# Kernel optimization log

Measured on AMD Instinct MI355X. Metric: run time of the kernel, lower is better.

## Reference

```python
import jax, jax.numpy as jnp
import numpy as np
import itertools, math

B = 2048
DIM = 384
RES = 7
KEY_DIM = 16
HEADS = 8
RATIO = 4
NH_KD = KEY_DIM * HEADS          # 128
D = RATIO * KEY_DIM              # 64
DH = D * HEADS                   # 512
OUT_DIM = DIM                    # 384
RES2 = math.ceil(RES / 2)        # 4
N = RES * RES                    # 49
N2 = RES2 * RES2                 # 16
EPS = 1e-5
SCALE = KEY_DIM ** -0.5


def conv2d(x, w, b, stride=1, pad=0, groups=1):
    out = jax.lax.conv_general_dilated(
        x, w, (stride, stride), [(pad, pad), (pad, pad)],
        dimension_numbers=("NCHW", "OIHW", "NCHW"), feature_group_count=groups)
    return out + b[None, :, None, None]


def bn(x, p):
    # p: [4, C] = (gamma, beta, running_mean, running_var); inference-mode BN
    g, be, m, v = p[0], p[1], p[2], p[3]
    inv = jax.lax.rsqrt(v + EPS)
    return (x - m[None, :, None, None]) * (g * inv)[None, :, None, None] + be[None, :, None, None]


def avgpool2(x):
    # AvgPool2d(kernel=2, stride=2, padding=0)
    s = jax.lax.reduce_window(x, 0.0, jax.lax.add, (1, 1, 2, 2), (1, 1, 2, 2), "VALID")
    return s * 0.25


def _bias_idxs():
    points = list(itertools.product(range(RES), range(RES)))
    points_ = list(itertools.product(range(RES2), range(RES2)))
    stride = RES / RES2
    offsets, idxs = {}, []
    for p1 in points_:
        for p2 in points:
            off = (math.floor(abs(p1[0] * stride - p2[0])),
                   math.floor(abs(p1[1] * stride - p2[1])))
            if off not in offsets:
                offsets[off] = len(offsets)
            idxs.append(offsets[off])
    return np.array(idxs, dtype=np.int32).reshape(N2, N), len(offsets)


def _bn_params(k, c):
    k1, k2, k3, k4 = jax.random.split(k, 4)
    gamma = 1.0 + 0.1 * jax.random.normal(k1, (c,), jnp.float32)
    beta = 0.1 * jax.random.normal(k2, (c,), jnp.float32)
    mean = 0.1 * jax.random.normal(k3, (c,), jnp.float32)
    var = jax.random.uniform(k4, (c,), jnp.float32, 0.5, 1.5)
    return jnp.stack([gamma, beta, mean, var])


def _conv_w(k, shape):
    fan_in = shape[1] * shape[2] * shape[3]
    return jax.random.normal(k, shape, jnp.float32) / np.sqrt(fan_in)


def setup_inputs() -> dict:
    key = jax.random.key(0)
    ks = jax.random.split(key, 20)
    idxs_np, n_off = _bias_idxs()
    inp = {
        "x": jax.random.normal(ks[0], (B, DIM, RES, RES), jnp.float32),
        # LGQuery: depthwise 3x3 s2 + proj 1x1 + BN
        "qlw": _conv_w(ks[1], (DIM, 1, 3, 3)),
        "qlb": 0.01 * jax.random.normal(ks[2], (DIM,), jnp.float32),
        "qpw": _conv_w(ks[3], (NH_KD, DIM, 1, 1)),
        "qpb": 0.01 * jax.random.normal(ks[4], (NH_KD,), jnp.float32),
        "qbn": _bn_params(ks[5], NH_KD),
        # K branch: 1x1 conv + BN
        "kw": _conv_w(ks[6], (NH_KD, DIM, 1, 1)),
        "kb": 0.01 * jax.random.normal(ks[7], (NH_KD,), jnp.float32),
        "kbn": _bn_params(ks[8], NH_KD),
        # V branch: 1x1 conv + BN
        "vw": _conv_w(ks[9], (DH, DIM, 1, 1)),
        "vb": 0.01 * jax.random.normal(ks[10], (DH,), jnp.float32),
        "vbn": _bn_params(ks[11], DH),
        # v_local: depthwise 3x3 s2 + BN
        "vlw": _conv_w(ks[12], (DH, 1, 3, 3)),
        "vlb": 0.01 * jax.random.normal(ks[13], (DH,), jnp.float32),
        "vlbn": _bn_params(ks[14], DH),
        # proj: ReLU -> 1x1 conv -> BN
        "pw": _conv_w(ks[15], (OUT_DIM, DH, 1, 1)),
        "pb": 0.01 * jax.random.normal(ks[16], (OUT_DIM,), jnp.float32),
        "pbn": _bn_params(ks[17], OUT_DIM),
        # relative position biases + gather indices
        "ab": 0.02 * jax.random.normal(ks[18], (HEADS, n_off), jnp.float32),
        "bias_idxs": jnp.asarray(idxs_np),
    }
    return inp


def reference(x, qlw, qlb, qpw, qpb, qbn, kw, kb, kbn, vw, vb, vbn,
              vlw, vlb, vlbn, pw, pb, pbn, ab, bias_idxs):
    Bx = x.shape[0]
    # --- LGQuery ---
    local_q = conv2d(x, qlw, qlb, stride=2, pad=1, groups=DIM)   # [B,384,4,4]
    pool_q = avgpool2(x)                                         # [B,384,3,3]
    ph = local_q.shape[-2] - pool_q.shape[-2]
    pw_ = local_q.shape[-1] - pool_q.shape[-1]
    if ph > 0 or pw_ > 0:
        pool_q = jnp.pad(pool_q, ((0, 0), (0, 0), (0, ph), (0, pw_)))
    q_out = bn(conv2d(local_q + pool_q, qpw, qpb), qbn)          # [B,128,4,4]
    Hq, Wq = q_out.shape[-2], q_out.shape[-1]
    Nq = Hq * Wq
    # --- K / V ---
    k_out = bn(conv2d(x, kw, kb), kbn)                           # [B,128,7,7]
    Nk = k_out.shape[-2] * k_out.shape[-1]
    v_out = bn(conv2d(x, vw, vb), vbn)                           # [B,512,7,7]
    v_loc = bn(conv2d(v_out, vlw, vlb, stride=2, pad=1, groups=DH), vlbn)  # [B,512,4,4]
    # --- attention over tiny 16x49 matrices per head ---
    q = q_out.reshape(Bx, HEADS, KEY_DIM, Nq)                    # [B,H,kd,Nq]
    k = k_out.reshape(Bx, HEADS, KEY_DIM, Nk)                    # [B,H,kd,Nk]
    v = v_out.reshape(Bx, HEADS, D, Nk)                          # [B,H,d,Nk]
    attn = jnp.einsum("bhdq,bhdk->bhqk", q, k) * SCALE           # [B,H,16,49]
    if Nq == N2 and Nk == N:
        attn = attn + ab[:, bias_idxs]                           # gather -> [H,16,49]
    attn = jax.nn.softmax(attn, axis=-1)
    xa = jnp.einsum("bhqk,bhdk->bhdq", attn, v)                  # [B,H,d,Nq]
    out = xa.reshape(Bx, DH, Hq, Wq)                             # [B,512,4,4]
    ph2 = out.shape[-2] - v_loc.shape[-2]
    pw2 = out.shape[-1] - v_loc.shape[-1]
    if ph2 > 0 or pw2 > 0:
        v_loc = jnp.pad(v_loc, ((0, 0), (0, 0), (0, ph2), (0, pw2)))
    out = out + v_loc
    out = bn(conv2d(jax.nn.relu(out), pw, pb), pbn)              # [B,384,4,4]
    return out
```

## Files before the change

### kernel.cpp

```cpp
#include <hip/hip_runtime.h>
#include <hip/hip_bf16.h>


#define DIMC 384
#define NPOS 49
#define NHKD 128
#define DHC  512
#define OUTC 384

#define OFF_KW  0
#define OFF_VW  49152
#define OFF_QPW 245760
#define OFF_PW  294912
#define W_TOT   491520

#define XS_OFF 0
#define R0_OFF 19208
#define R1_OFF 27528
#define R2_OFF 32648
#define SMEM_ELEMS 40840

typedef __attribute__((ext_vector_type(8))) __bf16 bf16x8;
typedef __attribute__((ext_vector_type(4))) float f32x4;

static __device__ __forceinline__ __hip_bfloat16 f2b(float x) { return __float2bfloat16(x); }
static __device__ __forceinline__ float b2f(__hip_bfloat16 x) { return __bfloat162float(x); }
static __device__ __forceinline__ bf16x8 ld8(const __hip_bfloat16* p) { return *(const bf16x8*)p; }
static __device__ __forceinline__ f32x4 fzero() {
  f32x4 z; z[0] = 0.f; z[1] = 0.f; z[2] = 0.f; z[3] = 0.f; return z;
}
static __device__ __forceinline__ bf16x8 bzero() {
  bf16x8 z;
  #pragma unroll
  for (int j = 0; j < 8; ++j) z[j] = (__bf16)0.0f;
  return z;
}

static __device__ __forceinline__ void bn_so(const float* bn, int C, int ch,
                                             float convb, float& s, float& o) {
  float g  = bn[ch];
  float be = bn[C + ch];
  float mu = bn[2*C + ch];
  float va = bn[3*C + ch];
  s = g * rsqrtf(va + 1e-5f);
  o = be + (convb - mu) * s;
}

__global__ void prep_weights(const float* __restrict__ kw, const float* __restrict__ vw,
                             const float* __restrict__ qpw, const float* __restrict__ pw,
                             __hip_bfloat16* __restrict__ wsb) {
  for (int i = blockIdx.x * blockDim.x + threadIdx.x; i < W_TOT; i += gridDim.x * blockDim.x) {
    float v;
    if (i < OFF_VW)       v = kw[i - OFF_KW];
    else if (i < OFF_QPW) v = vw[i - OFF_VW];
    else if (i < OFF_PW)  v = qpw[i - OFF_QPW];
    else                  v = pw[i - OFF_PW];
    wsb[i] = f2b(v);
  }
}

__global__ __launch_bounds__(512, 4) void attn4d_kernel(
    const float* __restrict__ x,
    const float* __restrict__ qlw, const float* __restrict__ qlb,
    const float* __restrict__ qpb, const float* __restrict__ qbn,
    const float* __restrict__ kb,  const float* __restrict__ kbn,
    const float* __restrict__ vb,  const float* __restrict__ vbn,
    const float* __restrict__ vlw, const float* __restrict__ vlb,
    const float* __restrict__ vlbn,
    const float* __restrict__ pb,  const float* __restrict__ pbn,
    const float* __restrict__ ab,  const int* __restrict__ bidx,
    const __hip_bfloat16* __restrict__ wsb,
    int n_off, float* __restrict__ out)
{
  __shared__ __align__(16) __hip_bfloat16 smem[SMEM_ELEMS];
  __hip_bfloat16* xs    = smem + XS_OFF;
  __hip_bfloat16* vsm   = smem + XS_OFF;
  __hip_bfloat16* kt    = smem + R0_OFF;
  __hip_bfloat16* rout  = smem + R0_OFF;
  __hip_bfloat16* qsm   = smem + R1_OFF;
  __hip_bfloat16* qin   = smem + R2_OFF;
  __hip_bfloat16* attnS = smem + R2_OFF;

  const __hip_bfloat16* kwb  = wsb + OFF_KW;
  const __hip_bfloat16* vwb  = wsb + OFF_VW;
  const __hip_bfloat16* qpwb = wsb + OFF_QPW;
  const __hip_bfloat16* pwb  = wsb + OFF_PW;

  const int tid  = threadIdx.x;
  const int lane = tid & 63;
  const int wave = tid >> 6;
  const int quad = lane >> 4;
  const int l15  = lane & 15;
  const int b    = blockIdx.x;

  {
    const float* xg = x + (size_t)b * (DIMC * NPOS);
    for (int j = tid; j < NPOS * (DIMC / 8); j += 512) {
      const int n  = j % 49;
      const int c0 = (j / 49) * 8;
      union { bf16x8 v; __hip_bfloat16 h[8]; } u;
      #pragma unroll
      for (int k = 0; k < 8; ++k)
        u.h[k] = f2b(xg[(c0 + k) * 49 + n]);
      *(bf16x8*)&xs[n * 392 + c0] = u.v;
    }
  }
  __syncthreads();

  if (tid < DIMC) {
    const int c = tid;
    float xv[49];
    #pragma unroll
    for (int n = 0; n < 49; ++n) xv[n] = b2f(xs[n * 392 + c]);
    float wq[9];
    #pragma unroll
    for (int j = 0; j < 9; ++j) wq[j] = qlw[c * 9 + j];
    const float cb = qlb[c];
    #pragma unroll
    for (int oh = 0; oh < 4; ++oh) {
      #pragma unroll
      for (int ow = 0; ow < 4; ++ow) {
        float a = cb;
        #pragma unroll
        for (int kh = 0; kh < 3; ++kh) {
          const int ih = 2 * oh - 1 + kh;
          if (ih < 0 || ih > 6) continue;
          #pragma unroll
          for (int kwi = 0; kwi < 3; ++kwi) {
            const int iw = 2 * ow - 1 + kwi;
            if (iw < 0 || iw > 6) continue;
            a += wq[kh * 3 + kwi] * xv[ih * 7 + iw];
          }
        }
        if (oh < 3 && ow < 3)
          a += 0.25f * (xv[(2*oh)*7 + 2*ow] + xv[(2*oh)*7 + 2*ow + 1] +
                        xv[(2*oh+1)*7 + 2*ow] + xv[(2*oh+1)*7 + 2*ow + 1]);
        qin[(oh * 4 + ow) * 392 + c] = f2b(a);
      }
    }
  }
  __syncthreads();


  {
    const int mt = wave;
    f32x4 acc[4];
    #pragma unroll
    for (int nt = 0; nt < 4; ++nt) acc[nt] = fzero();
    for (int ks = 0; ks < 12; ++ks) {
      const int c0 = ks * 32 + quad * 8;
      bf16x8 a = ld8(&kwb[(mt * 16 + l15) * DIMC + c0]);
      bf16x8 z[4];
      #pragma unroll
      for (int nt = 0; nt < 3; ++nt) z[nt] = ld8(&xs[(nt * 16 + l15) * 392 + c0]);
      z[3] = (l15 == 0) ? ld8(&xs[48 * 392 + c0]) : bzero();
      #pragma unroll
      for (int nt = 0; nt < 4; ++nt)
        acc[nt] = __builtin_amdgcn_mfma_f32_16x16x32_bf16(a, z[nt], acc[nt], 0, 0, 0);
    }
    #pragma unroll
    for (int r = 0; r < 4; ++r) {
      const int oc = mt * 16 + quad * 4 + r;
      float s, o;
      bn_so(kbn, NHKD, oc, kb[oc], s, o);
      #pragma unroll
      for (int nt = 0; nt < 4; ++nt) {
        const int n = nt * 16 + l15;
        if (n < 49) kt[n * 136 + oc] = f2b(acc[nt][r] * s + o);
      }
    }
  }

  {
    const int mt = wave;
    f32x4 acc = fzero();
    for (int ks = 0; ks < 12; ++ks) {
      const int c0 = ks * 32 + quad * 8;
      bf16x8 bv = ld8(&qin[l15 * 392 + c0]);
      bf16x8 av = ld8(&qpwb[(mt * 16 + l15) * DIMC + c0]);
      acc = __builtin_amdgcn_mfma_f32_16x16x32_bf16(av, bv, acc, 0, 0, 0);
    }
    #pragma unroll
    for (int r = 0; r < 4; ++r) {
      const int oc = mt * 16 + quad * 4 + r;
      float s, o;
      bn_so(qbn, NHKD, oc, qpb[oc], s, o);
      const int kd = oc & 15;
      qsm[wave * 640 + l15 * 40 + kd] = f2b(acc[r] * s + o);
      qsm[wave * 640 + l15 * 40 + kd + 16] = f2b(0.f);
    }
  }

  f32x4 va[2][2][4];
  #pragma unroll
  for (int p = 0; p < 2; ++p)
    #pragma unroll
    for (int mt = 0; mt < 2; ++mt)
      #pragma unroll
      for (int nt = 0; nt < 4; ++nt) va[p][mt][nt] = fzero();
  {
    const int chb = wave * 32;
    for (int ks = 0; ks < 12; ++ks) {
      const int c0 = ks * 32 + quad * 8;
      bf16x8 z[4];
      #pragma unroll
      for (int nt = 0; nt < 3; ++nt) z[nt] = ld8(&xs[(nt * 16 + l15) * 392 + c0]);
      z[3] = (l15 == 0) ? ld8(&xs[48 * 392 + c0]) : bzero();
      #pragma unroll
      for (int p = 0; p < 2; ++p) {
        #pragma unroll
        for (int mt = 0; mt < 2; ++mt) {
          bf16x8 a = ld8(&vwb[(p * 256 + chb + mt * 16 + l15) * DIMC + c0]);
          #pragma unroll
          for (int nt = 0; nt < 4; ++nt)
            va[p][mt][nt] = __builtin_amdgcn_mfma_f32_16x16x32_bf16(a, z[nt], va[p][mt][nt], 0, 0, 0);
        }
      }
    }
  }
  __syncthreads();

  {
    __hip_bfloat16* vbw_ = vsm + wave * 2304;
    #pragma unroll
    for (int mt = 0; mt < 2; ++mt)
      #pragma unroll
      for (int r = 0; r < 4; ++r) {
        const int chl = mt * 16 + quad * 4 + r;
        const int gch = wave * 32 + chl;
        float s, o;
        bn_so(vbn, DHC, gch, vb[gch], s, o);
        #pragma unroll
        for (int nt = 0; nt < 4; ++nt)
          vbw_[chl * 72 + nt * 16 + l15] = f2b(va[0][mt][nt][r] * s + o);
      }
  }

  {
    const int h = wave;
    bf16x8 av = ld8(&qsm[h * 640 + l15 * 40 + quad * 8]);
    float p[4][4];
    #pragma unroll
    for (int t = 0; t < 4; ++t) {
      bf16x8 bv = bzero();
      if (quad < 2) bv = ld8(&kt[(t * 16 + l15) * 136 + h * 16 + quad * 8]);
      f32x4 lg = __builtin_amdgcn_mfma_f32_16x16x32_bf16(av, bv, fzero(), 0, 0, 0);
      #pragma unroll
      for (int r = 0; r < 4; ++r) {
        const int nq = quad * 4 + r;
        const int nk = t * 16 + l15;
        float val = -30000.f;
        if (nk < 49) val = lg[r] * 0.25f + ab[h * n_off + bidx[nq * 49 + nk]];
        p[t][r] = val;
      }
    }
    #pragma unroll
    for (int r = 0; r < 4; ++r) {
      float m = fmaxf(fmaxf(p[0][r], p[1][r]), fmaxf(p[2][r], p[3][r]));
      m = fmaxf(m, __shfl_xor(m, 1));
      m = fmaxf(m, __shfl_xor(m, 2));
      m = fmaxf(m, __shfl_xor(m, 4));
      m = fmaxf(m, __shfl_xor(m, 8));
      float e[4], sum = 0.f;
      #pragma unroll
      for (int t = 0; t < 4; ++t) { e[t] = __expf(p[t][r] - m); sum += e[t]; }
      sum += __shfl_xor(sum, 1);
      sum += __shfl_xor(sum, 2);
      sum += __shfl_xor(sum, 4);
      sum += __shfl_xor(sum, 8);
      const float inv = 1.f / sum;
      #pragma unroll
      for (int t = 0; t < 4; ++t) p[t][r] = e[t] * inv;
    }
    #pragma unroll
    for (int r = 0; r < 4; ++r) {
      const int nq = quad * 4 + r;
      #pragma unroll
      for (int t = 0; t < 4; ++t) {
        const int nk = t * 16 + l15;
        attnS[h * 1024 + nq * 64 + (nk ^ ((nq & 7) << 3))] = f2b(p[t][r]);
      }
    }
  }
  __syncthreads();

  #pragma unroll
  for (int p = 0; p < 2; ++p) {
    if (p == 1) {
      __hip_bfloat16* vbw_ = vsm + wave * 2304;
      #pragma unroll
      for (int mt = 0; mt < 2; ++mt)
        #pragma unroll
        for (int r = 0; r < 4; ++r) {
          const int chl = mt * 16 + quad * 4 + r;
          const int gch = 256 + wave * 32 + chl;
          float s, o;
          bn_so(vbn, DHC, gch, vb[gch], s, o);
          #pragma unroll
          for (int nt = 0; nt < 4; ++nt)
            vbw_[chl * 72 + nt * 16 + l15] = f2b(va[1][mt][nt][r] * s + o);
        }
    }

    {
      const int cl   = lane & 31;
      const int half = lane >> 5;
      const int gch  = p * 256 + wave * 32 + cl;
      const __hip_bfloat16* vrow = vsm + wave * 2304 + cl * 72;
      float wv[9];
      #pragma unroll
      for (int j = 0; j < 9; ++j) wv[j] = vlw[gch * 9 + j];
      float s, o;
      bn_so(vlbn, DHC, gch, vlb[gch], s, o);
      #pragma unroll
      for (int pp = 0; pp < 8; ++pp) {
        const int pos = half * 8 + pp;
        const int oh = pos >> 2, ow = pos & 3;
        float a = 0.f;
        #pragma unroll
        for (int kh = 0; kh < 3; ++kh) {
          const int ih = 2 * oh - 1 + kh;
          if (ih < 0 || ih > 6) continue;
          #pragma unroll
          for (int kwi = 0; kwi < 3; ++kwi) {
            const int iw = 2 * ow - 1 + kwi;
            if (iw < 0 || iw > 6) continue;
            a += wv[kh * 3 + kwi] * b2f(vrow[ih * 7 + iw]);
          }
        }
        rout[pos * 520 + gch] = f2b(a * s + o);
      }
    }

    {
      const int h = p * 4 + (wave >> 1);
      const __hip_bfloat16* vbw_ = vsm + wave * 2304;
      #pragma unroll
      for (int mt = 0; mt < 2; ++mt) {
        f32x4 acc = fzero();
        #pragma unroll
        for (int ks = 0; ks < 2; ++ks) {
          const int k0 = ks * 32 + quad * 8;
          bf16x8 av = ld8(&vbw_[(mt * 16 + l15) * 72 + k0]);
          bf16x8 bv = ld8(&attnS[h * 1024 + l15 * 64 + (k0 ^ ((l15 & 7) << 3))]);
          acc = __builtin_amdgcn_mfma_f32_16x16x32_bf16(av, bv, acc, 0, 0, 0);
        }
        #pragma unroll
        for (int r = 0; r < 4; ++r) {
          const int gch = p * 256 + wave * 32 + mt * 16 + quad * 4 + r;
          const int ad = l15 * 520 + gch;
          const float val = acc[r] + b2f(rout[ad]);
          rout[ad] = f2b(fmaxf(val, 0.f));
        }
      }
    }
  }
  __syncthreads();

  {
    const int mt0 = wave * 3;
    f32x4 acc[3];
    #pragma unroll
    for (int t = 0; t < 3; ++t) acc[t] = fzero();
    for (int ks = 0; ks < 16; ++ks) {
      const int c0 = ks * 32 + quad * 8;
      bf16x8 bv = ld8(&rout[l15 * 520 + c0]);
      #pragma unroll
      for (int t = 0; t < 3; ++t) {
        bf16x8 av = ld8(&pwb[((mt0 + t) * 16 + l15) * DHC + c0]);
        acc[t] = __builtin_amdgcn_mfma_f32_16x16x32_bf16(av, bv, acc[t], 0, 0, 0);
      }
    }
    float* outb = out + (size_t)b * (OUTC * 16);
    #pragma unroll
    for (int t = 0; t < 3; ++t) {
      #pragma unroll
      for (int r = 0; r < 4; ++r) {
        const int oc = (mt0 + t) * 16 + quad * 4 + r;
        float s, o;
        bn_so(pbn, OUTC, oc, pb[oc], s, o);
        outb[oc * 16 + l15] = acc[t][r] * s + o;
      }
    }
  }
}

extern "C" void kernel_launch(void* const* d_in, const int* in_sizes, int n_in,
                              void* d_out, int out_size, void* d_ws, size_t ws_size,
                              hipStream_t stream) {
  const float* x    = (const float*)d_in[0];
  const float* qlw  = (const float*)d_in[1];
  const float* qlb  = (const float*)d_in[2];
  const float* qpw  = (const float*)d_in[3];
  const float* qpb  = (const float*)d_in[4];
  const float* qbn  = (const float*)d_in[5];
  const float* kw   = (const float*)d_in[6];
  const float* kb   = (const float*)d_in[7];
  const float* kbn  = (const float*)d_in[8];
  const float* vw   = (const float*)d_in[9];
  const float* vb   = (const float*)d_in[10];
  const float* vbn  = (const float*)d_in[11];
  const float* vlw  = (const float*)d_in[12];
  const float* vlb  = (const float*)d_in[13];
  const float* vlbn = (const float*)d_in[14];
  const float* pw   = (const float*)d_in[15];
  const float* pb   = (const float*)d_in[16];
  const float* pbn  = (const float*)d_in[17];
  const float* ab   = (const float*)d_in[18];
  const int*   bidx = (const int*)d_in[19];
  const int n_off = in_sizes[18] / 8;
  const int Bn = in_sizes[0] / (DIMC * NPOS);

  __hip_bfloat16* wsb = (__hip_bfloat16*)d_ws;

  prep_weights<<<480, 256, 0, stream>>>(kw, vw, qpw, pw, wsb);
  attn4d_kernel<<<Bn, 512, 0, stream>>>(x, qlw, qlb, qpb, qbn, kb, kbn,
                                        vb, vbn, vlw, vlb, vlbn, pb, pbn,
                                        ab, bidx, wsb, n_off, (float*)d_out);
}
```

Before: 580.2 us.

## Double block to 1024 threads, repartition GEMMs, precompute BN scale/offset tables

Raises the per-sample block from 512 to 1024 threads and redistributes every stage (q-path conv split by rows, K/V projections split across n-tiles and channel groups, attention on waves 8-15 overlapping with the v-local depthwise conv, output projection over 16 waves). All of V is kept in a separate, larger shared-memory region so the two-pass V handling goes away. BN scale/offset pairs are folded once in the prep kernel and stored in the workspace, replacing per-thread rsqrt and loads. Shared memory grows to about 156 KB per block, which limits residency to one block per CU and may reduce latency hiding.

```diff
diff --git a/kernel.cpp b/kernel.cpp
--- a/kernel.cpp
+++ b/kernel.cpp
@@ -13,12 +13,19 @@
 #define OFF_QPW 245760
 #define OFF_PW  294912
 #define W_TOT   491520
-
-#define XS_OFF 0
-#define R0_OFF 19208
-#define R1_OFF 27528
-#define R2_OFF 32648
-#define SMEM_ELEMS 40840
+#define BN_K  0
+#define BN_Q  128
+#define BN_V  256
+#define BN_VL 768
+#define BN_P  1280
+#define BN_TOT 1664
+
+#define XS_OFF   0
+#define KT_OFF   19208
+#define QSM_OFF  27912
+#define QIN_OFF  33032
+#define VSM_OFF  41224
+#define SMEM_ELEMS 78088
 
 typedef __attribute__((ext_vector_type(8))) __bf16 bf16x8;
 typedef __attribute__((ext_vector_type(4))) float f32x4;
@@ -36,20 +43,17 @@
   return z;
 }
 
-static __device__ __forceinline__ void bn_so(const float* bn, int C, int ch,
-                                             float convb, float& s, float& o) {
-  float g  = bn[ch];
-  float be = bn[C + ch];
-  float mu = bn[2*C + ch];
-  float va = bn[3*C + ch];
-  s = g * rsqrtf(va + 1e-5f);
-  o = be + (convb - mu) * s;
-}
-
 __global__ void prep_weights(const float* __restrict__ kw, const float* __restrict__ vw,
                              const float* __restrict__ qpw, const float* __restrict__ pw,
+                             const float* __restrict__ kb,  const float* __restrict__ kbn,
+                             const float* __restrict__ qpb, const float* __restrict__ qbn,
+                             const float* __restrict__ vb,  const float* __restrict__ vbn,
+                             const float* __restrict__ vlb, const float* __restrict__ vlbn,
+                             const float* __restrict__ pb,  const float* __restrict__ pbn,
                              __hip_bfloat16* __restrict__ wsb) {
-  for (int i = blockIdx.x * blockDim.x + threadIdx.x; i < W_TOT; i += gridDim.x * blockDim.x) {
+  const int gid = blockIdx.x * blockDim.x + threadIdx.x;
+  const int stride = gridDim.x * blockDim.x;
+  for (int i = gid; i < W_TOT; i += stride) {
     float v;
     if (i < OFF_VW)       v = kw[i - OFF_KW];
     else if (i < OFF_QPW) v = vw[i - OFF_VW];
@@ -57,34 +61,42 @@
     else                  v = pw[i - OFF_PW];
     wsb[i] = f2b(v);
   }
-}
-
-__global__ __launch_bounds__(512, 4) void attn4d_kernel(
+  float2* bnt = (float2*)(wsb + W_TOT);
+  for (int i = gid; i < BN_TOT; i += stride) {
+    const float *bn, *cb; int ch, C;
+    if (i < BN_Q)        { bn = kbn;  cb = kb;  ch = i;         C = NHKD; }
+    else if (i < BN_V)   { bn = qbn;  cb = qpb; ch = i - BN_Q;  C = NHKD; }
+    else if (i < BN_VL)  { bn = vbn;  cb = vb;  ch = i - BN_V;  C = DHC;  }
+    else if (i < BN_P)   { bn = vlbn; cb = vlb; ch = i - BN_VL; C = DHC;  }
+    else                 { bn = pbn;  cb = pb;  ch = i - BN_P;  C = OUTC; }
+    const float g = bn[ch], be = bn[C + ch], mu = bn[2*C + ch], va = bn[3*C + ch];
+    const float s = g * rsqrtf(va + 1e-5f);
+    bnt[i] = make_float2(s, be + (cb[ch] - mu) * s);
+  }
+}
+
+__global__ __launch_bounds__(1024, 4) void attn4d_kernel(
     const float* __restrict__ x,
     const float* __restrict__ qlw, const float* __restrict__ qlb,
-    const float* __restrict__ qpb, const float* __restrict__ qbn,
-    const float* __restrict__ kb,  const float* __restrict__ kbn,
-    const float* __restrict__ vb,  const float* __restrict__ vbn,
-    const float* __restrict__ vlw, const float* __restrict__ vlb,
-    const float* __restrict__ vlbn,
-    const float* __restrict__ pb,  const float* __restrict__ pbn,
+    const float* __restrict__ vlw,
     const float* __restrict__ ab,  const int* __restrict__ bidx,
     const __hip_bfloat16* __restrict__ wsb,
     int n_off, float* __restrict__ out)
 {
   __shared__ __align__(16) __hip_bfloat16 smem[SMEM_ELEMS];
   __hip_bfloat16* xs    = smem + XS_OFF;
-  __hip_bfloat16* vsm   = smem + XS_OFF;
-  __hip_bfloat16* kt    = smem + R0_OFF;
-  __hip_bfloat16* rout  = smem + R0_OFF;
-  __hip_bfloat16* qsm   = smem + R1_OFF;
-  __hip_bfloat16* qin   = smem + R2_OFF;
-  __hip_bfloat16* attnS = smem + R2_OFF;
+  __hip_bfloat16* rout  = smem + XS_OFF;
+  __hip_bfloat16* kt    = smem + KT_OFF;
+  __hip_bfloat16* qsm   = smem + QSM_OFF;
+  __hip_bfloat16* qin   = smem + QIN_OFF;
+  __hip_bfloat16* attnS = smem + QIN_OFF;
+  __hip_bfloat16* vsm   = smem + VSM_OFF;
 
   const __hip_bfloat16* kwb  = wsb + OFF_KW;
   const __hip_bfloat16* vwb  = wsb + OFF_VW;
   const __hip_bfloat16* qpwb = wsb + OFF_QPW;
   const __hip_bfloat16* pwb  = wsb + OFF_PW;
+  const float2* bnt = (const float2*)(wsb + W_TOT);
 
   const int tid  = threadIdx.x;
   const int lane = tid & 63;
@@ -95,7 +107,7 @@
 
   {
     const float* xg = x + (size_t)b * (DIMC * NPOS);
-    for (int j = tid; j < NPOS * (DIMC / 8); j += 512) {
+    for (int j = tid; j < NPOS * (DIMC / 8); j += 1024) {
       const int n  = j % 49;
       const int c0 = (j / 49) * 8;
       union { bf16x8 v; __hip_bfloat16 h[8]; } u;
@@ -107,17 +119,20 @@
   }
   __syncthreads();
 
-  if (tid < DIMC) {
-    const int c = tid;
-    float xv[49];
-    #pragma unroll
-    for (int n = 0; n < 49; ++n) xv[n] = b2f(xs[n * 392 + c]);
+  if (tid < 768) {
+    const int part = tid >= 384;
+    const int c    = tid - part * 384;
+    const int nb   = part * 21;
+    float xv[28];
+    #pragma unroll
+    for (int i = 0; i < 28; ++i) xv[i] = b2f(xs[(nb + i) * 392 + c]);
     float wq[9];
     #pragma unroll
     for (int j = 0; j < 9; ++j) wq[j] = qlw[c * 9 + j];
     const float cb = qlb[c];
     #pragma unroll
-    for (int oh = 0; oh < 4; ++oh) {
+    for (int ohh = 0; ohh < 2; ++ohh) {
+      const int oh = part * 2 + ohh;
       #pragma unroll
       for (int ow = 0; ow < 4; ++ow) {
         float a = cb;
@@ -129,12 +144,12 @@
           for (int kwi = 0; kwi < 3; ++kwi) {
             const int iw = 2 * ow - 1 + kwi;
             if (iw < 0 || iw > 6) continue;
-            a += wq[kh * 3 + kwi] * xv[ih * 7 + iw];
+            a += wq[kh * 3 + kwi] * xv[ih * 7 + iw - nb];
           }
         }
         if (oh < 3 && ow < 3)
-          a += 0.25f * (xv[(2*oh)*7 + 2*ow] + xv[(2*oh)*7 + 2*ow + 1] +
-                        xv[(2*oh+1)*7 + 2*ow] + xv[(2*oh+1)*7 + 2*ow + 1]);
+          a += 0.25f * (xv[(2*oh)*7 + 2*ow - nb]   + xv[(2*oh)*7 + 2*ow + 1 - nb] +
+                        xv[(2*oh+1)*7 + 2*ow - nb] + xv[(2*oh+1)*7 + 2*ow + 1 - nb]);
         qin[(oh * 4 + ow) * 392 + c] = f2b(a);
       }
     }
@@ -143,35 +158,30 @@
 
 
   {
-    const int mt = wave;
-    f32x4 acc[4];
-    #pragma unroll
-    for (int nt = 0; nt < 4; ++nt) acc[nt] = fzero();
+    const int nt  = wave & 3;
+    const int mtp = wave >> 2;
+    const int n   = nt * 16 + l15;
+    f32x4 acc[2]; acc[0] = fzero(); acc[1] = fzero();
     for (int ks = 0; ks < 12; ++ks) {
       const int c0 = ks * 32 + quad * 8;
-      bf16x8 a = ld8(&kwb[(mt * 16 + l15) * DIMC + c0]);
-      bf16x8 z[4];
-      #pragma unroll
-      for (int nt = 0; nt < 3; ++nt) z[nt] = ld8(&xs[(nt * 16 + l15) * 392 + c0]);
-      z[3] = (l15 == 0) ? ld8(&xs[48 * 392 + c0]) : bzero();
-      #pragma unroll
-      for (int nt = 0; nt < 4; ++nt)
-        acc[nt] = __builtin_amdgcn_mfma_f32_16x16x32_bf16(a, z[nt], acc[nt], 0, 0, 0);
-    }
-    #pragma unroll
-    for (int r = 0; r < 4; ++r) {
-      const int oc = mt * 16 + quad * 4 + r;
-      float s, o;
-      bn_so(kbn, NHKD, oc, kb[oc], s, o);
-      #pragma unroll
-      for (int nt = 0; nt < 4; ++nt) {
-        const int n = nt * 16 + l15;
-        if (n < 49) kt[n * 136 + oc] = f2b(acc[nt][r] * s + o);
-      }
-    }
-  }
-
-  {
+      bf16x8 z = (n < 49) ? ld8(&xs[n * 392 + c0]) : bzero();
+      #pragma unroll
+      for (int i = 0; i < 2; ++i) {
+        bf16x8 a = ld8(&kwb[((mtp * 2 + i) * 16 + l15) * DIMC + c0]);
+        acc[i] = __builtin_amdgcn_mfma_f32_16x16x32_bf16(a, z, acc[i], 0, 0, 0);
+      }
+    }
+    #pragma unroll
+    for (int i = 0; i < 2; ++i)
+      #pragma unroll
+      for (int r = 0; r < 4; ++r) {
+        const int oc = (mtp * 2 + i) * 16 + quad * 4 + r;
+        const float2 so = bnt[BN_K + oc];
+        if (n < 49) kt[n * 136 + oc] = f2b(acc[i][r] * so.x + so.y);
+      }
+  }
+
+  if (wave < 8) {
     const int mt = wave;
     f32x4 acc = fzero();
     for (int ks = 0; ks < 12; ++ks) {
@@ -183,61 +193,42 @@
     #pragma unroll
     for (int r = 0; r < 4; ++r) {
       const int oc = mt * 16 + quad * 4 + r;
-      float s, o;
-      bn_so(qbn, NHKD, oc, qpb[oc], s, o);
+      const float2 so = bnt[BN_Q + oc];
       const int kd = oc & 15;
-      qsm[wave * 640 + l15 * 40 + kd] = f2b(acc[r] * s + o);
+      qsm[wave * 640 + l15 * 40 + kd] = f2b(acc[r] * so.x + so.y);
       qsm[wave * 640 + l15 * 40 + kd + 16] = f2b(0.f);
     }
   }
 
-  f32x4 va[2][2][4];
-  #pragma unroll
-  for (int p = 0; p < 2; ++p)
-    #pragma unroll
-    for (int mt = 0; mt < 2; ++mt)
-      #pragma unroll
-      for (int nt = 0; nt < 4; ++nt) va[p][mt][nt] = fzero();
-  {
-    const int chb = wave * 32;
+  {
+    const int nt   = wave >> 2;
+    const int mgrp = wave & 3;
+    const int n    = nt * 16 + l15;
+    f32x4 va[8];
+    #pragma unroll
+    for (int i = 0; i < 8; ++i) va[i] = fzero();
     for (int ks = 0; ks < 12; ++ks) {
       const int c0 = ks * 32 + quad * 8;
-      bf16x8 z[4];
-      #pragma unroll
-      for (int nt = 0; nt < 3; ++nt) z[nt] = ld8(&xs[(nt * 16 + l15) * 392 + c0]);
-      z[3] = (l15 == 0) ? ld8(&xs[48 * 392 + c0]) : bzero();
-      #pragma unroll
-      for (int p = 0; p < 2; ++p) {
-        #pragma unroll
-        for (int mt = 0; mt < 2; ++mt) {
-          bf16x8 a = ld8(&vwb[(p * 256 + chb + mt * 16 + l15) * DIMC + c0]);
-          #pragma unroll
-          for (int nt = 0; nt < 4; ++nt)
-            va[p][mt][nt] = __builtin_amdgcn_mfma_f32_16x16x32_bf16(a, z[nt], va[p][mt][nt], 0, 0, 0);
-        }
-      }
-    }
-  }
-  __syncthreads();
-
-  {
-    __hip_bfloat16* vbw_ = vsm + wave * 2304;
-    #pragma unroll
-    for (int mt = 0; mt < 2; ++mt)
-      #pragma unroll
-      for (int r = 0; r < 4; ++r) {
-        const int chl = mt * 16 + quad * 4 + r;
-        const int gch = wave * 32 + chl;
-        float s, o;
-        bn_so(vbn, DHC, gch, vb[gch], s, o);
-        #pragma unroll
-        for (int nt = 0; nt < 4; ++nt)
-          vbw_[chl * 72 + nt * 16 + l15] = f2b(va[0][mt][nt][r] * s + o);
-      }
-  }
-
-  {
-    const int h = wave;
+      bf16x8 z = (n < 49) ? ld8(&xs[n * 392 + c0]) : bzero();
+      #pragma unroll
+      for (int i = 0; i < 8; ++i) {
+        bf16x8 a = ld8(&vwb[((mgrp * 8 + i) * 16 + l15) * DIMC + c0]);
+        va[i] = __builtin_amdgcn_mfma_f32_16x16x32_bf16(a, z, va[i], 0, 0, 0);
+      }
+    }
+    #pragma unroll
+    for (int i = 0; i < 8; ++i)
+      #pragma unroll
+      for (int r = 0; r < 4; ++r) {
+        const int ch = (mgrp * 8 + i) * 16 + quad * 4 + r;
+        const float2 so = bnt[BN_V + ch];
+        vsm[ch * 72 + n] = f2b(va[i][r] * so.x + so.y);
+      }
+  }
+  __syncthreads();
+
+  if (wave >= 8) {
+    const int h = wave - 8;
     bf16x8 av = ld8(&qsm[h * 640 + l15 * 40 + quad * 8]);
     float p[4][4];
     #pragma unroll
@@ -282,104 +273,91 @@
       }
     }
   }
-  __syncthreads();
-
-  #pragma unroll
-  for (int p = 0; p < 2; ++p) {
-    if (p == 1) {
-      __hip_bfloat16* vbw_ = vsm + wave * 2304;
-      #pragma unroll
-      for (int mt = 0; mt < 2; ++mt)
+
+  {
+    const int cl   = lane & 31;
+    const int half = lane >> 5;
+    const int gch  = wave * 32 + cl;
+    const __hip_bfloat16* vrow = vsm + gch * 72;
+    bf16x8 rv[7];
+    #pragma unroll
+    for (int t = 0; t < 7; ++t) rv[t] = ld8(vrow + t * 8);
+    float wv[9];
+    #pragma unroll
+    for (int j = 0; j < 9; ++j) wv[j] = vlw[gch * 9 + j];
+    const float2 so = bnt[BN_VL + gch];
+    #pragma unroll
+    for (int pp = 0; pp < 8; ++pp) {
+      const int pos = half * 8 + pp;
+      const int oh = pos >> 2, ow = pos & 3;
+      float a = 0.f;
+      #pragma unroll
+      for (int kh = 0; kh < 3; ++kh) {
+        const int ih = 2 * oh - 1 + kh;
+        if (ih < 0 || ih > 6) continue;
         #pragma unroll
-        for (int r = 0; r < 4; ++r) {
-          const int chl = mt * 16 + quad * 4 + r;
-          const int gch = 256 + wave * 32 + chl;
-          float s, o;
-          bn_so(vbn, DHC, gch, vb[gch], s, o);
-          #pragma unroll
-          for (int nt = 0; nt < 4; ++nt)
-            vbw_[chl * 72 + nt * 16 + l15] = f2b(va[1][mt][nt][r] * s + o);
+        for (int kwi = 0; kwi < 3; ++kwi) {
+          const int iw = 2 * ow - 1 + kwi;
+          if (iw < 0 || iw > 6) continue;
+          const int e = ih * 7 + iw;
+          a += wv[kh * 3 + kwi] * (float)rv[e >> 3][e & 7];
         }
-    }
-
-    {
-      const int cl   = lane & 31;
-      const int half = lane >> 5;
-      const int gch  = p * 256 + wave * 32 + cl;
-      const __hip_bfloat16* vrow = vsm + wave * 2304 + cl * 72;
-      float wv[9];
-      #pragma unroll
-      for (int j = 0; j < 9; ++j) wv[j] = vlw[gch * 9 + j];
-      float s, o;
-      bn_so(vlbn, DHC, gch, vlb[gch], s, o);
-      #pragma unroll
-      for (int pp = 0; pp < 8; ++pp) {
-        const int pos = half * 8 + pp;
-        const int oh = pos >> 2, ow = pos & 3;
-        float a = 0.f;
-        #pragma unroll
-        for (int kh = 0; kh < 3; ++kh) {
-          const int ih = 2 * oh - 1 + kh;
-          if (ih < 0 || ih > 6) continue;
-          #pragma unroll
-          for (int kwi = 0; kwi < 3; ++kwi) {
-            const int iw = 2 * ow - 1 + kwi;
-            if (iw < 0 || iw > 6) continue;
-            a += wv[kh * 3 + kwi] * b2f(vrow[ih * 7 + iw]);
-          }
-        }
-        rout[pos * 520 + gch] = f2b(a * s + o);
-      }
-    }
-
-    {
-      const int h = p * 4 + (wave >> 1);
-      const __hip_bfloat16* vbw_ = vsm + wave * 2304;
-      #pragma unroll
-      for (int mt = 0; mt < 2; ++mt) {
-        f32x4 acc = fzero();
-        #pragma unroll
-        for (int ks = 0; ks < 2; ++ks) {
-          const int k0 = ks * 32 + quad * 8;
-          bf16x8 av = ld8(&vbw_[(mt * 16 + l15) * 72 + k0]);
-          bf16x8 bv = ld8(&attnS[h * 1024 + l15 * 64 + (k0 ^ ((l15 & 7) << 3))]);
-          acc = __builtin_amdgcn_mfma_f32_16x16x32_bf16(av, bv, acc, 0, 0, 0);
-        }
-        #pragma unroll
-        for (int r = 0; r < 4; ++r) {
-          const int gch = p * 256 + wave * 32 + mt * 16 + quad * 4 + r;
-          const int ad = l15 * 520 + gch;
-          const float val = acc[r] + b2f(rout[ad]);
-          rout[ad] = f2b(fmaxf(val, 0.f));
-        }
-      }
-    }
-  }
-  __syncthreads();
-
-  {
-    const int mt0 = wave * 3;
-    f32x4 acc[3];
-    #pragma unroll
-    for (int t = 0; t < 3; ++t) acc[t] = fzero();
+      }
+      rout[pos * 520 + gch] = f2b(a * so.x + so.y);
+    }
+  }
+  __syncthreads();
+
+  {
+    const int h   = wave >> 1;
+    const int ch0 = wave * 32;
+    f32x4 pacc[2]; pacc[0] = fzero(); pacc[1] = fzero();
+    #pragma unroll
+    for (int mt2 = 0; mt2 < 2; ++mt2)
+      #pragma unroll
+      for (int ks = 0; ks < 2; ++ks) {
+        const int k0 = ks * 32 + quad * 8;
+        bf16x8 avv = ld8(&vsm[(ch0 + mt2 * 16 + l15) * 72 + k0]);
+        bf16x8 bvv = ld8(&attnS[h * 1024 + l15 * 64 + (k0 ^ ((l15 & 7) << 3))]);
+        pacc[mt2] = __builtin_amdgcn_mfma_f32_16x16x32_bf16(avv, bvv, pacc[mt2], 0, 0, 0);
+      }
+    #pragma unroll
+    for (int mt2 = 0; mt2 < 2; ++mt2)
+      #pragma unroll
+      for (int r = 0; r < 4; ++r) {
+        const int ch = ch0 + mt2 * 16 + quad * 4 + r;
+        const int ad = l15 * 520 + ch;
+        const float val = pacc[mt2][r] + b2f(rout[ad]);
+        rout[ad] = f2b(fmaxf(val, 0.f));
+      }
+  }
+  __syncthreads();
+
+  {
+    f32x4 acc[2]; acc[0] = fzero(); acc[1] = fzero();
     for (int ks = 0; ks < 16; ++ks) {
       const int c0 = ks * 32 + quad * 8;
       bf16x8 bv = ld8(&rout[l15 * 520 + c0]);
-      #pragma unroll
-      for (int t = 0; t < 3; ++t) {
-        bf16x8 av = ld8(&pwb[((mt0 + t) * 16 + l15) * DHC + c0]);
-        acc[t] = __builtin_amdgcn_mfma_f32_16x16x32_bf16(av, bv, acc[t], 0, 0, 0);
+      bf16x8 av = ld8(&pwb[(wave * 16 + l15) * DHC + c0]);
+      acc[0] = __builtin_amdgcn_mfma_f32_16x16x32_bf16(av, bv, acc[0], 0, 0, 0);
+      if (wave < 8) {
+        bf16x8 av2 = ld8(&pwb[((16 + wave) * 16 + l15) * DHC + c0]);
+        acc[1] = __builtin_amdgcn_mfma_f32_16x16x32_bf16(av2, bv, acc[1], 0, 0, 0);
       }
     }
     float* outb = out + (size_t)b * (OUTC * 16);
     #pragma unroll
-    for (int t = 0; t < 3; ++t) {
-      #pragma unroll
-      for (int r = 0; r < 4; ++r) {
-        const int oc = (mt0 + t) * 16 + quad * 4 + r;
-        float s, o;
-        bn_so(pbn, OUTC, oc, pb[oc], s, o);
-        outb[oc * 16 + l15] = acc[t][r] * s + o;
+    for (int r = 0; r < 4; ++r) {
+      const int oc = wave * 16 + quad * 4 + r;
+      const float2 so = bnt[BN_P + oc];
+      outb[oc * 16 + l15] = acc[0][r] * so.x + so.y;
+    }
+    if (wave < 8) {
+      #pragma unroll
+      for (int r = 0; r < 4; ++r) {
+        const int oc = (16 + wave) * 16 + quad * 4 + r;
+        const float2 so = bnt[BN_P + oc];
+        outb[oc * 16 + l15] = acc[1][r] * so.x + so.y;
       }
     }
   }
@@ -413,8 +391,9 @@
 
   __hip_bfloat16* wsb = (__hip_bfloat16*)d_ws;
 
-  prep_weights<<<480, 256, 0, stream>>>(kw, vw, qpw, pw, wsb);
-  attn4d_kernel<<<Bn, 512, 0, stream>>>(x, qlw, qlb, qpb, qbn, kb, kbn,
-                                        vb, vbn, vlw, vlb, vlbn, pb, pbn,
-                                        ab, bidx, wsb, n_off, (float*)d_out);
-}
+  prep_weights<<<480, 256, 0, stream>>>(kw, vw, qpw, pw,
+                                        kb, kbn, qpb, qbn, vb, vbn,
+                                        vlb, vlbn, pb, pbn, wsb);
+  attn4d_kernel<<<Bn, 1024, 0, stream>>>(x, qlw, qlb, vlw, ab, bidx,
+                                         wsb, n_off, (float*)d_out);
+}
```

Result: slower. 1.035 ms (+78.4%).
